# Optimization experiments

Hardware: AMD Instinct MI355X
Metric: run time of the kernel (lower is better)

## Reference

```python
import jax, jax.numpy as jnp
import numpy as np

HIDDEN = 1024
RANK = 4
N_TASKS = 5
LORA_SCALING = 1.0 / RANK  # lora_alpha / lora_rank = 1/4
LN_EPS = 1e-5


def setup_inputs() -> dict:
    key = jax.random.key(0)
    ks = jax.random.split(key, 9)
    B, S, D = 16, 2048, HIDDEN
    hidden_states = jax.random.normal(ks[0], (B, S, D), dtype=jnp.float32)
    input_tensor = jax.random.normal(ks[1], (B, S, D), dtype=jnp.float32)
    adapter_mask = jax.random.randint(ks[2], (B,), 0, N_TASKS, dtype=jnp.int32)
    W = jax.random.normal(ks[3], (D, D), dtype=jnp.float32) * 0.02
    b = jax.random.normal(ks[4], (D,), dtype=jnp.float32) * 0.02
    lora_A = jax.random.normal(ks[5], (N_TASKS, RANK, D), dtype=jnp.float32) * 0.02
    lora_B = jax.random.normal(ks[6], (N_TASKS, D, RANK), dtype=jnp.float32) * 0.02
    gamma = jnp.ones((D,), dtype=jnp.float32)
    beta = jnp.zeros((D,), dtype=jnp.float32)
    return {
        "hidden_states": hidden_states,
        "input_tensor": input_tensor,
        "W": W,
        "b": b,
        "lora_A": lora_A,
        "lora_B": lora_B,
        "gamma": gamma,
        "beta": beta,
        "adapter_mask": adapter_mask,
    }


def _layernorm(x, gamma, beta):
    mu = jnp.mean(x, axis=-1, keepdims=True)
    xc = x - mu
    var = jnp.mean(xc * xc, axis=-1, keepdims=True)
    return xc * jax.lax.rsqrt(var + LN_EPS) * gamma + beta


def reference(hidden_states, input_tensor, W, b, lora_A, lora_B, gamma, beta, adapter_mask):
    # Base dense projection (first self.dense call)
    h1 = jnp.einsum("bsd,ed->bse", hidden_states, W) + b  # [B,S,D]
    # Per-task LoRA-parametrized dense applied to the projected states
    # (the source loops over unique tasks with gather/scatter; vectorized here
    #  by gathering each batch row's adapter).
    base2 = jnp.einsum("bsd,ed->bse", h1, W) + b  # [B,S,D]
    A_b = lora_A[adapter_mask]  # [B, r, D]
    B_b = lora_B[adapter_mask]  # [B, D, r]
    low = jnp.einsum("bsd,brd->bsr", h1, A_b)  # [B,S,r]
    delta = jnp.einsum("bsr,bdr->bsd", low, B_b)  # [B,S,D]
    h2 = base2 + LORA_SCALING * delta
    # dropout is identity in eval / p=0; residual + LayerNorm
    return _layernorm(h2 + input_tensor, gamma, beta)
```

## Files before the change

### kernel.cpp

```cpp
#include <hip/hip_runtime.h>
#include <hip/hip_bf16.h>
#include <stdint.h>

#define D_HID 1024
#define M_TOT 32768
#define LN_EPS 1e-5f

typedef __bf16 bf16x8 __attribute__((ext_vector_type(8)));
typedef float f32x4 __attribute__((ext_vector_type(4)));
typedef unsigned short u16;
typedef u16 u16x8 __attribute__((ext_vector_type(8)));
typedef u16 u16x4v __attribute__((ext_vector_type(4)));

__device__ __forceinline__ float bf2f(u16 x) {
  union { unsigned int u; float f; } c; c.u = ((unsigned int)x) << 16; return c.f;
}
__device__ __forceinline__ u16 f2bf(float f) {
  union { __bf16 h; u16 u; } c; c.h = (__bf16)f; return c.u;
}
__device__ __forceinline__ u16x8 cvt8(const float* g) {
  float4 f0 = *(const float4*)g;
  float4 f1 = *(const float4*)(g + 4);
  u16x8 v;
  v[0] = f2bf(f0.x); v[1] = f2bf(f0.y); v[2] = f2bf(f0.z); v[3] = f2bf(f0.w);
  v[4] = f2bf(f1.x); v[5] = f2bf(f1.y); v[6] = f2bf(f1.z); v[7] = f2bf(f1.w);
  return v;
}
__device__ __forceinline__ void gld16(const u16* g, u16* lds_wave_base) {
  __builtin_amdgcn_global_load_lds(
      (__attribute__((address_space(1))) unsigned int*)g,
      (__attribute__((address_space(3))) unsigned int*)lds_wave_base, 16, 0, 0);
}

__global__ __launch_bounds__(256) void s1_prep(
    const float* __restrict__ hs, u16* __restrict__ hs_bf,
    const float* __restrict__ W, u16* __restrict__ hi, u16* __restrict__ lo,
    u16* __restrict__ hiT, u16* __restrict__ loT) {
  __shared__ float tile[32][33];
  const int bid = blockIdx.x, tid = threadIdx.x;
  if (bid < 2048) {
    int i = bid * 256 + tid;
#pragma unroll
    for (int it = 0; it < 8; ++it, i += 2048 * 256)
      *(u16x8*)(hs_bf + (size_t)i * 8) = cvt8(hs + (size_t)i * 8);
    return;
  }
  const int rb = bid - 2048;
  const int bj = rb & 31, bi = rb >> 5;
  const int tx = tid & 31, ty = tid >> 5;
#pragma unroll
  for (int r0 = 0; r0 < 32; r0 += 8) {
    const int r = r0 + ty;
    const size_t o = (size_t)(bi * 32 + r) * D_HID + bj * 32 + tx;
    const float v = W[o];
    tile[r][tx] = v;
    const u16 h = f2bf(v);
    hi[o] = h; lo[o] = f2bf(v - bf2f(h));
  }
  __syncthreads();
#pragma unroll
  for (int r0 = 0; r0 < 32; r0 += 8) {
    const int r = r0 + ty;
    const float v = tile[tx][r];
    const size_t o = (size_t)(bj * 32 + r) * D_HID + bi * 32 + tx;
    const u16 h = f2bf(v);
    hiT[o] = h; loT[o] = f2bf(v - bf2f(h));
  }
}

__global__ __launch_bounds__(256, 1) void s2_wc_a2c(
    const u16* __restrict__ Ah, const u16* __restrict__ Al,
    const u16* __restrict__ Bh, const u16* __restrict__ Bl,
    const float* __restrict__ lA, float* __restrict__ C,
    float* __restrict__ A2) {
  __shared__ __align__(16) u16 sAh[128 * 32], sAl[128 * 32];
  __shared__ __align__(16) u16 sBh[128 * 32], sBl[128 * 32];
  const int bid = blockIdx.x, tid = threadIdx.x, wave = tid >> 6, lane = tid & 63;
  if (bid >= 64) {
    const int job = (bid - 64) * 4 + wave;
    const int tr = job >> 10, e = job & 1023;
    const u16* ht = Bh + (size_t)e * D_HID + lane * 16;
    const u16* lt = Bl + (size_t)e * D_HID + lane * 16;
    const float* ar = lA + (size_t)tr * D_HID + lane * 16;
    u16x8 h0 = *(const u16x8*)ht, h1 = *(const u16x8*)(ht + 8);
    u16x8 l0 = *(const u16x8*)lt, l1 = *(const u16x8*)(lt + 8);
    float acc = 0.f;
#pragma unroll
    for (int j = 0; j < 8; ++j) {
      acc += ar[j]     * (bf2f(h0[j]) + bf2f(l0[j]));
      acc += ar[8 + j] * (bf2f(h1[j]) + bf2f(l1[j]));
    }
#pragma unroll
    for (int m = 1; m < 64; m <<= 1) acc += __shfl_xor(acc, m);
    if (lane == 0) A2[(size_t)tr * D_HID + e] = acc;
    return;
  }
  const int bx = bid & 7, by = bid >> 3;
  const int srow = tid >> 2, scol = (tid & 3) * 8;
  size_t aOff = (size_t)(by * 128 + srow) * D_HID + scol;
  size_t bOff = (size_t)(bx * 128 + srow) * D_HID + scol;
  const int wb = wave * 512;
  const int wm = wave >> 1, wn = wave & 1;
  const int mrow = lane & 15, quad = lane >> 4;
  const int fA = (wm * 64 + mrow) * 32 + quad * 8;
  const int fB = (wn * 64 + mrow) * 32 + quad * 8;
  f32x4 acc[4][4];
#pragma unroll
  for (int i = 0; i < 4; ++i)
#pragma unroll
    for (int j = 0; j < 4; ++j) acc[i][j] = (f32x4){0.f, 0.f, 0.f, 0.f};
  for (int k0 = 0; k0 < D_HID; k0 += 32) {
    __syncthreads();
    gld16(Ah + aOff, sAh + wb); gld16(Ah + aOff + 64 * D_HID, sAh + wb + 2048);
    gld16(Al + aOff, sAl + wb); gld16(Al + aOff + 64 * D_HID, sAl + wb + 2048);
    gld16(Bh + bOff, sBh + wb); gld16(Bh + bOff + 64 * D_HID, sBh + wb + 2048);
    gld16(Bl + bOff, sBl + wb); gld16(Bl + bOff + 64 * D_HID, sBl + wb + 2048);
    aOff += 32; bOff += 32;
    __syncthreads();
    bf16x8 ah[4], al4[4], bh[4], bl4[4];
#pragma unroll
    for (int m = 0; m < 4; ++m) {
      ah[m]  = *(const bf16x8*)(sAh + fA + m * 512);
      al4[m] = *(const bf16x8*)(sAl + fA + m * 512);
    }
#pragma unroll
    for (int n = 0; n < 4; ++n) {
      bh[n]  = *(const bf16x8*)(sBh + fB + n * 512);
      bl4[n] = *(const bf16x8*)(sBl + fB + n * 512);
    }
#pragma unroll
    for (int m = 0; m < 4; ++m)
#pragma unroll
      for (int n = 0; n < 4; ++n) {
        acc[m][n] = __builtin_amdgcn_mfma_f32_16x16x32_bf16(ah[m],  bh[n],  acc[m][n], 0, 0, 0);
        acc[m][n] = __builtin_amdgcn_mfma_f32_16x16x32_bf16(al4[m], bh[n],  acc[m][n], 0, 0, 0);
        acc[m][n] = __builtin_amdgcn_mfma_f32_16x16x32_bf16(ah[m],  bl4[n], acc[m][n], 0, 0, 0);
      }
  }
  const int mBase = by * 128 + wm * 64, nBase = bx * 128 + wn * 64;
#pragma unroll
  for (int m = 0; m < 4; ++m)
#pragma unroll
    for (int n = 0; n < 4; ++n) {
      const int nn = nBase + n * 16 + mrow;
#pragma unroll
      for (int r = 0; r < 4; ++r)
        C[(size_t)(mBase + m * 16 + quad * 4 + r) * D_HID + nn] = acc[m][n][r];
    }
}

__global__ __launch_bounds__(256) void weff_beff(
    const float* __restrict__ Wc, const float* __restrict__ A2,
    const float* __restrict__ lB, const float* __restrict__ lA,
    const float* __restrict__ W, const float* __restrict__ bvec,
    u16* __restrict__ Weff, float* __restrict__ beff) {
  const int n = blockIdx.x, t = blockIdx.y, tid = threadIdx.x;
  const int wave = tid >> 6, lane = tid & 63;
  float br[4];
#pragma unroll
  for (int r = 0; r < 4; ++r) br[r] = lB[(size_t)t * 4096 + n * 4 + r];
  float4 v = *(const float4*)(Wc + (size_t)n * D_HID + tid * 4);
#pragma unroll
  for (int r = 0; r < 4; ++r) {
    const float4 a2 = *(const float4*)(A2 + (size_t)(t * 4 + r) * D_HID + tid * 4);
    const float s = 0.25f * br[r];
    v.x += s * a2.x; v.y += s * a2.y; v.z += s * a2.z; v.w += s * a2.w;
  }
  u16x4v o; o[0] = f2bf(v.x); o[1] = f2bf(v.y); o[2] = f2bf(v.z); o[3] = f2bf(v.w);
  *(u16x4v*)(Weff + (size_t)t * 1048576 + (size_t)n * D_HID + tid * 4) = o;
  const float4 bb = *(const float4*)(bvec + tid * 4);
  float p[5];
  {
    const float4 wr = *(const float4*)(W + (size_t)n * D_HID + tid * 4);
    p[0] = wr.x * bb.x + wr.y * bb.y + wr.z * bb.z + wr.w * bb.w;
  }
#pragma unroll
  for (int r = 0; r < 4; ++r) {
    const float4 ar = *(const float4*)(lA + (size_t)(t * 4 + r) * D_HID + tid * 4);
    p[1 + r] = ar.x * bb.x + ar.y * bb.y + ar.z * bb.z + ar.w * bb.w;
  }
#pragma unroll
  for (int m = 1; m < 64; m <<= 1)
#pragma unroll
    for (int j = 0; j < 5; ++j) p[j] += __shfl_xor(p[j], m);
  __shared__ float red[4][5];
  if (lane == 0)
#pragma unroll
    for (int j = 0; j < 5; ++j) red[wave][j] = p[j];
  __syncthreads();
  if (tid == 0) {
    float P = 0.f, Cr[4] = {0.f, 0.f, 0.f, 0.f};
#pragma unroll
    for (int w = 0; w < 4; ++w) {
      P += red[w][0];
#pragma unroll
      for (int r = 0; r < 4; ++r) Cr[r] += red[w][1 + r];
    }
    float e = 0.f;
#pragma unroll
    for (int r = 0; r < 4; ++r) e += br[r] * Cr[r];
    beff[t * D_HID + n] = P + bvec[n] + 0.25f * e;
  }
}

__global__ __launch_bounds__(256, 3) void gemm_main(
    const u16* __restrict__ A, const u16* __restrict__ Wf,
    const float* __restrict__ beff, const float* __restrict__ resid,
    const int* __restrict__ mask, float* __restrict__ out) {
  __shared__ __align__(16) u16 sA[2][128 * 32], sB[2][128 * 32];
  const int tid = threadIdx.x, wave = tid >> 6, lane = tid & 63;
  const int L = blockIdx.x + 8 * blockIdx.y;
  const int by = (L & 7) * 32 + (L >> 6);
  const int bx = (L >> 3) & 7;
  const int task = mask[by >> 4];
  const u16* Bt = Wf + (size_t)task * (D_HID * D_HID);
  const int srow = tid >> 2;
  const int scol = ((tid & 3) ^ (srow & 3)) * 8;
  size_t aOff = (size_t)(by * 128 + srow) * D_HID + scol;
  size_t bOff = (size_t)(bx * 128 + srow) * D_HID + scol;
  const int wb = wave * 512;
  const int wm = wave >> 1, wn = wave & 1;
  const int mrow = lane & 15, quad = lane >> 4;
  const int fA = (wm * 64 + mrow) * 32 + ((quad ^ (mrow & 3)) * 8);
  const int fB = (wn * 64 + mrow) * 32 + ((quad ^ (mrow & 3)) * 8);
  f32x4 acc[4][4];
#pragma unroll
  for (int i = 0; i < 4; ++i)
#pragma unroll
    for (int j = 0; j < 4; ++j) acc[i][j] = (f32x4){0.f, 0.f, 0.f, 0.f};

  auto stage = [&](int buf) {
    gld16(A + aOff,               &sA[buf][wb]);
    gld16(A + aOff + 64 * D_HID,  &sA[buf][wb + 2048]);
    gld16(Bt + bOff,              &sB[buf][wb]);
    gld16(Bt + bOff + 64 * D_HID, &sB[buf][wb + 2048]);
    aOff += 32; bOff += 32;
  };

  stage(0);
  __syncthreads();
  int cur = 0;
  for (int t = 0; t < 32; ++t) {
    if (t < 31) stage(cur ^ 1);
    bf16x8 af[4], bfr[4];
#pragma unroll
    for (int m = 0; m < 4; ++m) af[m]  = *(const bf16x8*)(&sA[cur][fA + m * 512]);
#pragma unroll
    for (int n = 0; n < 4; ++n) bfr[n] = *(const bf16x8*)(&sB[cur][fB + n * 512]);
#pragma unroll
    for (int m = 0; m < 4; ++m)
#pragma unroll
      for (int n = 0; n < 4; ++n)
        acc[m][n] = __builtin_amdgcn_mfma_f32_16x16x32_bf16(af[m], bfr[n], acc[m][n], 0, 0, 0);
    __syncthreads();
    cur ^= 1;
  }

  const float* bb = beff + task * D_HID;
  const size_t mBase = (size_t)by * 128 + wm * 64;
  const int nBase = bx * 128 + wn * 64;
#pragma unroll
  for (int mf = 0; mf < 4; ++mf)
#pragma unroll
    for (int nf = 0; nf < 4; ++nf) {
      const int n = nBase + nf * 16 + mrow;
      const float bval = bb[n];
#pragma unroll
      for (int r = 0; r < 4; ++r) {
        const size_t m = mBase + mf * 16 + quad * 4 + r;
        out[m * D_HID + n] = acc[mf][nf][r] + bval + resid[m * D_HID + n];
      }
    }
}

__global__ __launch_bounds__(256) void ln4(float* __restrict__ io,
                                           const float* __restrict__ gamma,
                                           const float* __restrict__ beta) {
  const int row = blockIdx.x * 4 + (threadIdx.x >> 6);
  const int lane = threadIdx.x & 63;
  float* p = io + (size_t)row * D_HID + lane * 16;
  float4 v0 = ((const float4*)p)[0], v1 = ((const float4*)p)[1];
  float4 v2 = ((const float4*)p)[2], v3 = ((const float4*)p)[3];
  float s = v0.x + v0.y + v0.z + v0.w + v1.x + v1.y + v1.z + v1.w
          + v2.x + v2.y + v2.z + v2.w + v3.x + v3.y + v3.z + v3.w;
  float q = v0.x*v0.x + v0.y*v0.y + v0.z*v0.z + v0.w*v0.w
          + v1.x*v1.x + v1.y*v1.y + v1.z*v1.z + v1.w*v1.w
          + v2.x*v2.x + v2.y*v2.y + v2.z*v2.z + v2.w*v2.w
          + v3.x*v3.x + v3.y*v3.y + v3.z*v3.z + v3.w*v3.w;
#pragma unroll
  for (int m = 1; m < 64; m <<= 1) { s += __shfl_xor(s, m); q += __shfl_xor(q, m); }
  const float mu  = s * (1.f / (float)D_HID);
  const float var = q * (1.f / (float)D_HID) - mu * mu;
  const float inv = rsqrtf(var + LN_EPS);
  const float4* gp = (const float4*)(gamma + lane * 16);
  const float4* bp = (const float4*)(beta + lane * 16);
  float4 g, bbv, o;
#define LNW(k, vk) \
  g = gp[k]; bbv = bp[k]; \
  o.x = (vk.x - mu) * inv * g.x + bbv.x; o.y = (vk.y - mu) * inv * g.y + bbv.y; \
  o.z = (vk.z - mu) * inv * g.z + bbv.z; o.w = (vk.w - mu) * inv * g.w + bbv.w; \
  ((float4*)p)[k] = o;
  LNW(0, v0) LNW(1, v1) LNW(2, v2) LNW(3, v3)
#undef LNW
}

extern "C" void kernel_launch(void* const* d_in, const int* in_sizes, int n_in,
                              void* d_out, int out_size, void* d_ws, size_t ws_size,
                              hipStream_t stream) {
  const float* hs    = (const float*)d_in[0];
  const float* inp   = (const float*)d_in[1];
  const float* W     = (const float*)d_in[2];
  const float* b     = (const float*)d_in[3];
  const float* lA    = (const float*)d_in[4];
  const float* lB    = (const float*)d_in[5];
  const float* gamma = (const float*)d_in[6];
  const float* beta  = (const float*)d_in[7];
  const int*   mask  = (const int*)d_in[8];
  float* out = (float*)d_out;

  char* wsb = (char*)d_ws;
  u16*   hs_bf = (u16*)wsb;
  float* Wc    = (float*)(wsb + 67108864);
  u16*   weff  = (u16*)(wsb + 71303168);
  u16*   Whi   = weff;
  u16*   Wlo   = weff + 1048576;
  u16*   WhiT  = weff + 2097152;
  u16*   WloT  = weff + 3145728;
  float* A2    = (float*)(wsb + 81788928);
  float* beff  = (float*)(wsb + 81871360);

  s1_prep<<<3072, 256, 0, stream>>>(hs, hs_bf, W, Whi, Wlo, WhiT, WloT);
  s2_wc_a2c<<<64 + 5120, 256, 0, stream>>>(Whi, Wlo, WhiT, WloT, lA, Wc, A2);
  weff_beff<<<dim3(1024, 5), 256, 0, stream>>>(Wc, A2, lB, lA, W, b, weff, beff);
  gemm_main<<<dim3(8, 256), 256, 0, stream>>>(hs_bf, weff, beff, inp, mask, out);
  ln4<<<M_TOT / 4, 256, 0, stream>>>(out, gamma, beta);
}
```

Before: 524.3 us.

## Triple-buffer main GEMM with explicit waitcnt pipeline and fold A2 into MFMA GEMM

The main GEMM moves from a double-buffered loop to a three-stage LDS ring. It uses explicit vmcnt waits, raw barriers, sched_barriers and setprio around the MFMA block, so global loads run two K-steps ahead. The LoRA A2 = lA·W product is no longer computed by 5120 per-wave dot-product blocks. Instead lA is split into bf16 hi/lo in the prep kernel and processed as an extra padded row-tile in the split-precision MFMA GEMM. The XOR swizzle on the LDS layout in gemm_main is dropped, which may bring back LDS bank conflicts, and the hand-written waitcnt counts must match the number of outstanding loads.

```diff
diff --git a/kernel.cpp b/kernel.cpp
--- a/kernel.cpp
+++ b/kernel.cpp
@@ -35,7 +35,8 @@
 __global__ __launch_bounds__(256) void s1_prep(
     const float* __restrict__ hs, u16* __restrict__ hs_bf,
     const float* __restrict__ W, u16* __restrict__ hi, u16* __restrict__ lo,
-    u16* __restrict__ hiT, u16* __restrict__ loT) {
+    u16* __restrict__ hiT, u16* __restrict__ loT,
+    const float* __restrict__ lA, u16* __restrict__ lAh, u16* __restrict__ lAl) {
   __shared__ float tile[32][33];
   const int bid = blockIdx.x, tid = threadIdx.x;
   if (bid < 2048) {
@@ -43,6 +44,17 @@
 #pragma unroll
     for (int it = 0; it < 8; ++it, i += 2048 * 256)
       *(u16x8*)(hs_bf + (size_t)i * 8) = cvt8(hs + (size_t)i * 8);
+    return;
+  }
+  if (bid >= 3072) {
+    const int b = bid - 3072;
+    for (int i = tid; i < 16 * 1024; i += 256) {
+      const int r = b * 16 + (i >> 10), c = i & 1023;
+      const float v = (r < 20) ? lA[(size_t)r * 1024 + c] : 0.f;
+      const u16 h = f2bf(v);
+      lAh[(size_t)r * 1024 + c] = h;
+      lAl[(size_t)r * 1024 + c] = f2bf(v - bf2f(h));
+    }
     return;
   }
   const int rb = bid - 2048;
@@ -68,34 +80,167 @@
   }
 }
 
-__global__ __launch_bounds__(256, 1) void s2_wc_a2c(
+__global__ __launch_bounds__(256, 1) void s2_gemm(
     const u16* __restrict__ Ah, const u16* __restrict__ Al,
     const u16* __restrict__ Bh, const u16* __restrict__ Bl,
-    const float* __restrict__ lA, float* __restrict__ C,
-    float* __restrict__ A2) {
+    const u16* __restrict__ lAh, const u16* __restrict__ lAl,
+    float* __restrict__ C, float* __restrict__ A2) {
   __shared__ __align__(16) u16 sAh[128 * 32], sAl[128 * 32];
   __shared__ __align__(16) u16 sBh[128 * 32], sBl[128 * 32];
   const int bid = blockIdx.x, tid = threadIdx.x, wave = tid >> 6, lane = tid & 63;
-  if (bid >= 64) {
-    const int job = (bid - 64) * 4 + wave;
-    const int tr = job >> 10, e = job & 1023;
-    const u16* ht = Bh + (size_t)e * D_HID + lane * 16;
-    const u16* lt = Bl + (size_t)e * D_HID + lane * 16;
-    const float* ar = lA + (size_t)tr * D_HID + lane * 16;
-    u16x8 h0 = *(const u16x8*)ht, h1 = *(const u16x8*)(ht + 8);
-    u16x8 l0 = *(const u16x8*)lt, l1 = *(const u16x8*)(lt + 8);
-    float acc = 0.f;
-#pragma unroll
-    for (int j = 0; j < 8; ++j) {
-      acc += ar[j]     * (bf2f(h0[j]) + bf2f(l0[j]));
-      acc += ar[8 + j] * (bf2f(h1[j]) + bf2f(l1[j]));
-    }
-#pragma unroll
-    for (int m = 1; m < 64; m <<= 1) acc += __shfl_xor(acc, m);
-    if (lane == 0) A2[(size_t)tr * D_HID + e] = acc;
-    return;
-  }
-  const int bx = bid & 7, by = bid >> 3;
+  const int by = bid >> 3, bx = bid & 7;
+  const bool isA2 = (by == 8);
+  const u16* Asrc_h = isA2 ? lAh : Ah;
+  const u16* Asrc_l = isA2 ? lAl : Al;
+  const int rowbase = isA2 ? 0 : by * 128;
+  const int srow = tid >> 2, scol = (tid & 3) * 8;
+  size_t aOff = (size_t)(rowbase + srow) * D_HID + scol;
+  size_t bOff = (size_t)(bx * 128 + srow) * D_HID + scol;
+  const int wb = wave * 512;
+  const int wm = wave >> 1, wn = wave & 1;
+  const int mrow = lane & 15, quad = lane >> 4;
+  const int fA = (wm * 64 + mrow) * 32 + quad * 8;
+  const int fB = (wn * 64 + mrow) * 32 + quad * 8;
+  f32x4 acc[4][4];
+#pragma unroll
+  for (int i = 0; i < 4; ++i)
+#pragma unroll
+    for (int j = 0; j < 4; ++j) acc[i][j] = (f32x4){0.f, 0.f, 0.f, 0.f};
+  for (int k0 = 0; k0 < D_HID; k0 += 32) {
+    __syncthreads();
+    gld16(Asrc_h + aOff, sAh + wb); gld16(Asrc_h + aOff + 64 * D_HID, sAh + wb + 2048);
+    gld16(Asrc_l + aOff, sAl + wb); gld16(Asrc_l + aOff + 64 * D_HID, sAl + wb + 2048);
+    gld16(Bh + bOff, sBh + wb); gld16(Bh + bOff + 64 * D_HID, sBh + wb + 2048);
+    gld16(Bl + bOff, sBl + wb); gld16(Bl + bOff + 64 * D_HID, sBl + wb + 2048);
+    aOff += 32; bOff += 32;
+    __syncthreads();
+    bf16x8 ah[4], al4[4], bh[4], bl4[4];
+#pragma unroll
+    for (int m = 0; m < 4; ++m) {
+      ah[m]  = *(const bf16x8*)(sAh + fA + m * 512);
+      al4[m] = *(const bf16x8*)(sAl + fA + m * 512);
+    }
+#pragma unroll
+    for (int n = 0; n < 4; ++n) {
+      bh[n]  = *(const bf16x8*)(sBh + fB + n * 512);
+      bl4[n] = *(const bf16x8*)(sBl + fB + n * 512);
+    }
+#pragma unroll
+    for (int m = 0; m < 4; ++m)
+#pragma unroll
+      for (int n = 0; n < 4; ++n) {
+        acc[m][n] = __builtin_amdgcn_mfma_f32_16x16x32_bf16(ah[m],  bh[n],  acc[m][n], 0, 0, 0);
+        acc[m][n] = __builtin_amdgcn_mfma_f32_16x16x32_bf16(al4[m], bh[n],  acc[m][n], 0, 0, 0);
+        acc[m][n] = __builtin_amdgcn_mfma_f32_16x16x32_bf16(ah[m],  bl4[n], acc[m][n], 0, 0, 0);
+      }
+  }
+  const int nBase = bx * 128 + wn * 64;
+#pragma unroll
+  for (int m = 0; m < 4; ++m)
+#pragma unroll
+    for (int n = 0; n < 4; ++n) {
+      const int nn = nBase + n * 16 + mrow;
+#pragma unroll
+      for (int r = 0; r < 4; ++r) {
+        const int lr = wm * 64 + m * 16 + quad * 4 + r;
+        if (!isA2) {
+          C[(size_t)(by * 128 + lr) * D_HID + nn] = acc[m][n][r];
+        } else if (lr < 20) {
+          A2[(size_t)lr * D_HID + nn] = acc[m][n][r];
+        }
+      }
+    }
+}
+
+__global__ __launch_bounds__(256) void weff_beff(
+    const float* __restrict__ Wc, const float* __restrict__ A2,
+    const float* __restrict__ lB, const float* __restrict__ lA,
+    const float* __restrict__ W, const float* __restrict__ bvec,
+    u16* __restrict__ Weff, float* __restrict__ beff) {
+  const int n = blockIdx.x, t = blockIdx.y, tid = threadIdx.x;
+  const int wave = tid >> 6, lane = tid & 63;
+  float br[4];
+#pragma unroll
+  for (int r = 0; r < 4; ++r) br[r] = lB[(size_t)t * 4096 + n * 4 + r];
+  float4 v = *(const float4*)(Wc + (size_t)n * D_HID + tid * 4);
+#pragma unroll
+  for (int r = 0; r < 4; ++r) {
+    const float4 a2 = *(const float4*)(A2 + (size_t)(t * 4 + r) * D_HID + tid * 4);
+    const float s = 0.25f * br[r];
+    v.x += s * a2.x; v.y += s * a2.y; v.z += s * a2.z; v.w += s * a2.w;
+  }
+  u16x4v o; o[0] = f2bf(v.x); o[1] = f2bf(v.y); o[2] = f2bf(v.z); o[3] = f2bf(v.w);
+  *(u16x4v*)(Weff + (size_t)t * 1048576 + (size_t)n * D_HID + tid * 4) = o;
+  const float4 bb = *(const float4*)(bvec + tid * 4);
+  float p[5];
+  {
+    const float4 wr = *(const float4*)(W + (size_t)n * D_HID + tid * 4);
+    p[0] = wr.x * bb.x + wr.y * bb.y + wr.z * bb.z + wr.w * bb.w;
+  }
+#pragma unroll
+  for (int r = 0; r < 4; ++r) {
+    const float4 ar = *(const float4*)(lA + (size_t)(t * 4 + r) * D_HID + tid * 4);
+    p[1 + r] = ar.x * bb.x + ar.y * bb.y + ar.z * bb.z + ar.w * bb.w;
+  }
+#pragma unroll
+  for (int m = 1; m < 64; m <<= 1)
+#pragma unroll
+    for (int j = 0; j < 5; ++j) p[j] += __shfl_xor(p[j], m);
+  __shared__ float red[4][5];
+  if (lane == 0)
+#pragma unroll
+    for (int j = 0; j < 5; ++j) red[wave][j] = p[j];
+  __syncthreads();
+  if (tid == 0) {
+    float P = 0.f, Cr[4] = {0.f, 0.f, 0.f, 0.f};
+#pragma unroll
+    for (int w = 0; w < 4; ++w) {
+      P += red[w][0];
+#pragma unroll
+      for (int r = 0; r < 4; ++r) Cr[r] += red[w][1 + r];
+    }
+    float e = 0.f;
+#pragma unroll
+    for (int r = 0; r < 4; ++r) e += br[r] * Cr[r];
+    beff[t * D_HID + n] = P + bvec[n] + 0.25f * e;
+  }
+}
+
+template <int VM>
+__device__ __forceinline__ void kstep(const u16* sAc, const u16* sBc,
+                                      int fA, int fB, f32x4 (&acc)[4][4]) {
+  asm volatile("s_waitcnt vmcnt(%0)" :: "n"(VM) : "memory");
+  __builtin_amdgcn_s_barrier();
+  __builtin_amdgcn_sched_barrier(0);
+  bf16x8 af[4], bfr[4];
+#pragma unroll
+  for (int m = 0; m < 4; ++m) af[m]  = *(const bf16x8*)(sAc + fA + m * 512);
+#pragma unroll
+  for (int n = 0; n < 4; ++n) bfr[n] = *(const bf16x8*)(sBc + fB + n * 512);
+  asm volatile("s_waitcnt lgkmcnt(0)" ::: "memory");
+  __builtin_amdgcn_sched_barrier(0);
+  __builtin_amdgcn_s_barrier();
+  __builtin_amdgcn_sched_barrier(0);
+  __builtin_amdgcn_s_setprio(1);
+#pragma unroll
+  for (int m = 0; m < 4; ++m)
+#pragma unroll
+    for (int n = 0; n < 4; ++n)
+      acc[m][n] = __builtin_amdgcn_mfma_f32_16x16x32_bf16(af[m], bfr[n], acc[m][n], 0, 0, 0);
+  __builtin_amdgcn_s_setprio(0);
+}
+
+__global__ __launch_bounds__(256, 3) void gemm_main(
+    const u16* __restrict__ A, const u16* __restrict__ Wf,
+    const float* __restrict__ beff, const float* __restrict__ resid,
+    const int* __restrict__ mask, float* __restrict__ out) {
+  __shared__ __align__(16) u16 sA[3][4096], sB[3][4096];
+  const int tid = threadIdx.x, wave = tid >> 6, lane = tid & 63;
+  const int L = blockIdx.x;
+  const int by = (L & 7) * 32 + (L >> 6);
+  const int bx = (L >> 3) & 7;
+  const int task = mask[by >> 4];
+  const u16* Bt = Wf + (size_t)task * (D_HID * D_HID);
   const int srow = tid >> 2, scol = (tid & 3) * 8;
   size_t aOff = (size_t)(by * 128 + srow) * D_HID + scol;
   size_t bOff = (size_t)(bx * 128 + srow) * D_HID + scol;
@@ -109,125 +254,6 @@
   for (int i = 0; i < 4; ++i)
 #pragma unroll
     for (int j = 0; j < 4; ++j) acc[i][j] = (f32x4){0.f, 0.f, 0.f, 0.f};
-  for (int k0 = 0; k0 < D_HID; k0 += 32) {
-    __syncthreads();
-    gld16(Ah + aOff, sAh + wb); gld16(Ah + aOff + 64 * D_HID, sAh + wb + 2048);
-    gld16(Al + aOff, sAl + wb); gld16(Al + aOff + 64 * D_HID, sAl + wb + 2048);
-    gld16(Bh + bOff, sBh + wb); gld16(Bh + bOff + 64 * D_HID, sBh + wb + 2048);
-    gld16(Bl + bOff, sBl + wb); gld16(Bl + bOff + 64 * D_HID, sBl + wb + 2048);
-    aOff += 32; bOff += 32;
-    __syncthreads();
-    bf16x8 ah[4], al4[4], bh[4], bl4[4];
-#pragma unroll
-    for (int m = 0; m < 4; ++m) {
-      ah[m]  = *(const bf16x8*)(sAh + fA + m * 512);
-      al4[m] = *(const bf16x8*)(sAl + fA + m * 512);
-    }
-#pragma unroll
-    for (int n = 0; n < 4; ++n) {
-      bh[n]  = *(const bf16x8*)(sBh + fB + n * 512);
-      bl4[n] = *(const bf16x8*)(sBl + fB + n * 512);
-    }
-#pragma unroll
-    for (int m = 0; m < 4; ++m)
-#pragma unroll
-      for (int n = 0; n < 4; ++n) {
-        acc[m][n] = __builtin_amdgcn_mfma_f32_16x16x32_bf16(ah[m],  bh[n],  acc[m][n], 0, 0, 0);
-        acc[m][n] = __builtin_amdgcn_mfma_f32_16x16x32_bf16(al4[m], bh[n],  acc[m][n], 0, 0, 0);
-        acc[m][n] = __builtin_amdgcn_mfma_f32_16x16x32_bf16(ah[m],  bl4[n], acc[m][n], 0, 0, 0);
-      }
-  }
-  const int mBase = by * 128 + wm * 64, nBase = bx * 128 + wn * 64;
-#pragma unroll
-  for (int m = 0; m < 4; ++m)
-#pragma unroll
-    for (int n = 0; n < 4; ++n) {
-      const int nn = nBase + n * 16 + mrow;
-#pragma unroll
-      for (int r = 0; r < 4; ++r)
-        C[(size_t)(mBase + m * 16 + quad * 4 + r) * D_HID + nn] = acc[m][n][r];
-    }
-}
-
-__global__ __launch_bounds__(256) void weff_beff(
-    const float* __restrict__ Wc, const float* __restrict__ A2,
-    const float* __restrict__ lB, const float* __restrict__ lA,
-    const float* __restrict__ W, const float* __restrict__ bvec,
-    u16* __restrict__ Weff, float* __restrict__ beff) {
-  const int n = blockIdx.x, t = blockIdx.y, tid = threadIdx.x;
-  const int wave = tid >> 6, lane = tid & 63;
-  float br[4];
-#pragma unroll
-  for (int r = 0; r < 4; ++r) br[r] = lB[(size_t)t * 4096 + n * 4 + r];
-  float4 v = *(const float4*)(Wc + (size_t)n * D_HID + tid * 4);
-#pragma unroll
-  for (int r = 0; r < 4; ++r) {
-    const float4 a2 = *(const float4*)(A2 + (size_t)(t * 4 + r) * D_HID + tid * 4);
-    const float s = 0.25f * br[r];
-    v.x += s * a2.x; v.y += s * a2.y; v.z += s * a2.z; v.w += s * a2.w;
-  }
-  u16x4v o; o[0] = f2bf(v.x); o[1] = f2bf(v.y); o[2] = f2bf(v.z); o[3] = f2bf(v.w);
-  *(u16x4v*)(Weff + (size_t)t * 1048576 + (size_t)n * D_HID + tid * 4) = o;
-  const float4 bb = *(const float4*)(bvec + tid * 4);
-  float p[5];
-  {
-    const float4 wr = *(const float4*)(W + (size_t)n * D_HID + tid * 4);
-    p[0] = wr.x * bb.x + wr.y * bb.y + wr.z * bb.z + wr.w * bb.w;
-  }
-#pragma unroll
-  for (int r = 0; r < 4; ++r) {
-    const float4 ar = *(const float4*)(lA + (size_t)(t * 4 + r) * D_HID + tid * 4);
-    p[1 + r] = ar.x * bb.x + ar.y * bb.y + ar.z * bb.z + ar.w * bb.w;
-  }
-#pragma unroll
-  for (int m = 1; m < 64; m <<= 1)
-#pragma unroll
-    for (int j = 0; j < 5; ++j) p[j] += __shfl_xor(p[j], m);
-  __shared__ float red[4][5];
-  if (lane == 0)
-#pragma unroll
-    for (int j = 0; j < 5; ++j) red[wave][j] = p[j];
-  __syncthreads();
-  if (tid == 0) {
-    float P = 0.f, Cr[4] = {0.f, 0.f, 0.f, 0.f};
-#pragma unroll
-    for (int w = 0; w < 4; ++w) {
-      P += red[w][0];
-#pragma unroll
-      for (int r = 0; r < 4; ++r) Cr[r] += red[w][1 + r];
-    }
-    float e = 0.f;
-#pragma unroll
-    for (int r = 0; r < 4; ++r) e += br[r] * Cr[r];
-    beff[t * D_HID + n] = P + bvec[n] + 0.25f * e;
-  }
-}
-
-__global__ __launch_bounds__(256, 3) void gemm_main(
-    const u16* __restrict__ A, const u16* __restrict__ Wf,
-    const float* __restrict__ beff, const float* __restrict__ resid,
-    const int* __restrict__ mask, float* __restrict__ out) {
-  __shared__ __align__(16) u16 sA[2][128 * 32], sB[2][128 * 32];
-  const int tid = threadIdx.x, wave = tid >> 6, lane = tid & 63;
-  const int L = blockIdx.x + 8 * blockIdx.y;
-  const int by = (L & 7) * 32 + (L >> 6);
-  const int bx = (L >> 3) & 7;
-  const int task = mask[by >> 4];
-  const u16* Bt = Wf + (size_t)task * (D_HID * D_HID);
-  const int srow = tid >> 2;
-  const int scol = ((tid & 3) ^ (srow & 3)) * 8;
-  size_t aOff = (size_t)(by * 128 + srow) * D_HID + scol;
-  size_t bOff = (size_t)(bx * 128 + srow) * D_HID + scol;
-  const int wb = wave * 512;
-  const int wm = wave >> 1, wn = wave & 1;
-  const int mrow = lane & 15, quad = lane >> 4;
-  const int fA = (wm * 64 + mrow) * 32 + ((quad ^ (mrow & 3)) * 8);
-  const int fB = (wn * 64 + mrow) * 32 + ((quad ^ (mrow & 3)) * 8);
-  f32x4 acc[4][4];
-#pragma unroll
-  for (int i = 0; i < 4; ++i)
-#pragma unroll
-    for (int j = 0; j < 4; ++j) acc[i][j] = (f32x4){0.f, 0.f, 0.f, 0.f};
 
   auto stage = [&](int buf) {
     gld16(A + aOff,               &sA[buf][wb]);
@@ -238,23 +264,17 @@
   };
 
   stage(0);
-  __syncthreads();
+  stage(1);
   int cur = 0;
-  for (int t = 0; t < 32; ++t) {
-    if (t < 31) stage(cur ^ 1);
-    bf16x8 af[4], bfr[4];
-#pragma unroll
-    for (int m = 0; m < 4; ++m) af[m]  = *(const bf16x8*)(&sA[cur][fA + m * 512]);
-#pragma unroll
-    for (int n = 0; n < 4; ++n) bfr[n] = *(const bf16x8*)(&sB[cur][fB + n * 512]);
-#pragma unroll
-    for (int m = 0; m < 4; ++m)
-#pragma unroll
-      for (int n = 0; n < 4; ++n)
-        acc[m][n] = __builtin_amdgcn_mfma_f32_16x16x32_bf16(af[m], bfr[n], acc[m][n], 0, 0, 0);
-    __syncthreads();
-    cur ^= 1;
-  }
+  for (int t = 0; t < 30; ++t) {
+    int sb = cur + 2; if (sb >= 3) sb -= 3;
+    stage(sb);
+    kstep<8>(&sA[cur][0], &sB[cur][0], fA, fB, acc);
+    if (++cur == 3) cur = 0;
+  }
+  kstep<4>(&sA[cur][0], &sB[cur][0], fA, fB, acc);
+  if (++cur == 3) cur = 0;
+  kstep<0>(&sA[cur][0], &sB[cur][0], fA, fB, acc);
 
   const float* bb = beff + task * D_HID;
   const size_t mBase = (size_t)by * 128 + wm * 64;
@@ -326,12 +346,14 @@
   u16*   Wlo   = weff + 1048576;
   u16*   WhiT  = weff + 2097152;
   u16*   WloT  = weff + 3145728;
+  u16*   lAh   = weff + 4194304;
+  u16*   lAl   = weff + 4325376;
   float* A2    = (float*)(wsb + 81788928);
   float* beff  = (float*)(wsb + 81871360);
 
-  s1_prep<<<3072, 256, 0, stream>>>(hs, hs_bf, W, Whi, Wlo, WhiT, WloT);
-  s2_wc_a2c<<<64 + 5120, 256, 0, stream>>>(Whi, Wlo, WhiT, WloT, lA, Wc, A2);
+  s1_prep<<<3080, 256, 0, stream>>>(hs, hs_bf, W, Whi, Wlo, WhiT, WloT, lA, lAh, lAl);
+  s2_gemm<<<72, 256, 0, stream>>>(Whi, Wlo, WhiT, WloT, lAh, lAl, Wc, A2);
   weff_beff<<<dim3(1024, 5), 256, 0, stream>>>(Wc, A2, lB, lA, W, b, weff, beff);
-  gemm_main<<<dim3(8, 256), 256, 0, stream>>>(hs_bf, weff, beff, inp, mask, out);
+  gemm_main<<<2048, 256, 0, stream>>>(hs_bf, weff, beff, inp, mask, out);
   ln4<<<M_TOT / 4, 256, 0, stream>>>(out, gamma, beta);
 }
```

Result: slower. 556.7 us (+6.2%).
